# Kernel tuning notes

Hardware: AMD Instinct MI355X
Metric: run time of the kernel (lower is better)

Reference implementation:

```python
import jax, jax.numpy as jnp
import numpy as np

B, T, C = 4, 1024, 512
H, HD = 8, 64
NE, K = 8, 2
FF = 4 * C


def setup_inputs() -> dict:
    key = jax.random.key(0)
    ks = jax.random.split(key, 16)
    s = 0.02
    return {
        "x": jax.random.normal(ks[0], (B, T, C), jnp.float32),
        "ln1_g": jnp.ones((C,), jnp.float32),
        "ln1_b": jnp.zeros((C,), jnp.float32),
        "ln2_g": jnp.ones((C,), jnp.float32),
        "ln2_b": jnp.zeros((C,), jnp.float32),
        "Wq": jax.random.normal(ks[1], (H, C, HD), jnp.float32) * s,
        "Wk": jax.random.normal(ks[2], (H, C, HD), jnp.float32) * s,
        "Wv": jax.random.normal(ks[3], (H, C, HD), jnp.float32) * s,
        "Wp": jax.random.normal(ks[4], (H * HD, C), jnp.float32) * s,
        "bp": jnp.zeros((C,), jnp.float32),
        "Wr": jax.random.normal(ks[5], (C, NE), jnp.float32) * s,
        "br": jnp.zeros((NE,), jnp.float32),
        "W1": jax.random.normal(ks[6], (NE, C, FF), jnp.float32) * s,
        "b1": jnp.zeros((NE, FF), jnp.float32),
        "W2": jax.random.normal(ks[7], (NE, FF, C), jnp.float32) * s,
        "b2": jnp.zeros((NE, C), jnp.float32),
    }


def _ln(x, g, b, eps=1e-5):
    mu = jnp.mean(x, axis=-1, keepdims=True)
    var = jnp.var(x, axis=-1, keepdims=True)
    return (x - mu) * jax.lax.rsqrt(var + eps) * g + b


def reference(x, ln1_g, ln1_b, ln2_g, ln2_b, Wq, Wk, Wv, Wp, bp, Wr, br, W1, b1, W2, b2):
    # --- multi-head causal attention (all heads stacked) ---
    h = _ln(x, ln1_g, ln1_b)
    q = jnp.einsum("btc,hcd->bhtd", h, Wq)
    k = jnp.einsum("btc,hcd->bhtd", h, Wk)
    v = jnp.einsum("btc,hcd->bhtd", h, Wv)
    wei = jnp.einsum("bhtd,bhsd->bhts", q, k) / np.sqrt(HD).astype(np.float32)
    causal = jnp.tril(jnp.ones((T, T), bool))
    wei = jnp.where(causal, wei, -jnp.inf)
    wei = jax.nn.softmax(wei, axis=-1)
    attn = jnp.einsum("bhts,bhsd->bhtd", wei, v)  # [B,H,T,HD]
    attn = attn.transpose(0, 2, 1, 3).reshape(B, T, H * HD)
    x2 = x + attn @ Wp + bp

    # --- SparseMoE: dense all-experts compute, masked top-k combine ---
    h2 = _ln(x2, ln2_g, ln2_b)
    scores = h2 @ Wr + br  # [B,T,NE]
    topk_scores, indices = jax.lax.top_k(scores, K)
    # scatter top-k scores into zeros (rest stays 0), then softmax over experts
    mask = jnp.sum(jax.nn.one_hot(indices, NE, dtype=scores.dtype) * topk_scores[..., None], axis=-2)
    router = jax.nn.softmax(mask, axis=-1)  # [B,T,NE]
    hid = jax.nn.relu(jnp.einsum("btc,ecf->btef", h2, W1) + b1)  # [B,T,NE,FF]
    eo = jnp.einsum("btef,efc->btec", hid, W2) + b2  # [B,T,NE,C]
    moe = jnp.einsum("bte,btec->btc", router, eo)
    return x2 + moe
```

## Files before the change

kernel.cpp:

```cpp
#include <hip/hip_runtime.h>


typedef unsigned short u16;
typedef __attribute__((ext_vector_type(8))) short s16x8;
typedef __attribute__((ext_vector_type(4))) float f32x4;

__device__ __forceinline__ u16 f2bf(float f) {
  union { float f; unsigned u; } v; v.f = f;
  unsigned r = v.u + 0x7fffu + ((v.u >> 16) & 1u);
  return (u16)(r >> 16);
}
__device__ __forceinline__ float bf2f(u16 h) {
  union { unsigned u; float f; } v; v.u = ((unsigned)h) << 16;
  return v.f;
}

#define GLDS16(g, s) __builtin_amdgcn_global_load_lds( \
    (const __attribute__((address_space(1))) void*)(g), \
    (__attribute__((address_space(3))) void*)(s), 16, 0, 0)

#define MFMA16(a, b, c) __builtin_amdgcn_mfma_f32_16x16x32_bf16((a), (b), (c), 0, 0, 0)

__global__ __launch_bounds__(256) void transpose_k(
    const float* __restrict__ in, u16* __restrict__ out,
    int R, int C, long long ibs, long long obs, float scale)
{
  __shared__ float tile[32][33];
  in  += (long long)blockIdx.z * ibs;
  out += (long long)blockIdx.z * obs;
  const int c0 = blockIdx.x * 32, r0 = blockIdx.y * 32;
  const int tx = threadIdx.x, ty = threadIdx.y;
  #pragma unroll
  for (int i = 0; i < 4; ++i)
    tile[ty + i*8][tx] = in[(size_t)(r0 + ty + i*8) * C + c0 + tx];
  __syncthreads();
  #pragma unroll
  for (int i = 0; i < 4; ++i)
    out[(size_t)(c0 + ty + i*8) * R + r0 + tx] = f2bf(tile[tx][ty + i*8] * scale);
}

__global__ __launch_bounds__(256) void transqkv_k(
    const float* __restrict__ Wq, const float* __restrict__ Wk,
    const float* __restrict__ Wv, const float* __restrict__ Wp,
    u16* __restrict__ oqkv, u16* __restrict__ owp)
{
  __shared__ float tile[32][33];
  const int z = blockIdx.z;
  const int tx = threadIdx.x, ty = threadIdx.y;
  if (z < 24) {
    const int which = z >> 3, head = z & 7;
    const float* in = (which == 0 ? Wq : (which == 1 ? Wk : Wv)) + (size_t)head * 512 * 64;
    u16* o = oqkv + (size_t)which * 512 * 512 + (size_t)head * 64 * 512;
    const float scale = (which == 0) ? 0.125f : 1.f;
    const int c0 = blockIdx.x * 32, r0 = blockIdx.y * 32;
    #pragma unroll
    for (int i = 0; i < 4; ++i)
      tile[ty + i*8][tx] = in[(size_t)(r0 + ty + i*8) * 64 + c0 + tx];
    __syncthreads();
    #pragma unroll
    for (int i = 0; i < 4; ++i)
      o[(size_t)(c0 + ty + i*8) * 512 + r0 + tx] = f2bf(tile[tx][ty + i*8] * scale);
  } else {
    const int zz = z - 24;
    const int c0 = (zz * 2 + blockIdx.x) * 32;
    const int r0 = blockIdx.y * 32;
    #pragma unroll
    for (int i = 0; i < 4; ++i)
      tile[ty + i*8][tx] = Wp[(size_t)(r0 + ty + i*8) * 512 + c0 + tx];
    __syncthreads();
    #pragma unroll
    for (int i = 0; i < 4; ++i)
      owp[(size_t)(c0 + ty + i*8) * 512 + r0 + tx] = f2bf(tile[tx][ty + i*8]);
  }
}

__global__ __launch_bounds__(256) void vtrans_k(
    const u16* __restrict__ qkv, u16* __restrict__ vt)
{
  __shared__ u16 tile[32][33];
  const int bh = blockIdx.z, b = bh >> 3, h = bh & 7;
  const int t0 = blockIdx.x * 32, d0 = blockIdx.y * 32;
  const int tx = threadIdx.x, ty = threadIdx.y;
  #pragma unroll
  for (int i = 0; i < 4; ++i)
    tile[ty + i*8][tx] = qkv[(size_t)(b*1024 + t0 + ty + i*8) * 1536 + 1024 + h*64 + d0 + tx];
  __syncthreads();
  #pragma unroll
  for (int i = 0; i < 4; ++i)
    vt[(size_t)bh*65536 + (size_t)(d0 + ty + i*8) * 1024 + t0 + tx] = tile[tx][ty + i*8];
}

__global__ __launch_bounds__(256) void ln_k(
    const float* __restrict__ x, const float* __restrict__ g,
    const float* __restrict__ b, u16* __restrict__ o)
{
  const int row = blockIdx.x, t = threadIdx.x;
  const float* xr = x + (size_t)row * 512;
  const float a0 = xr[t], a1 = xr[t + 256];
  float s = a0 + a1, ss = a0*a0 + a1*a1;
  #pragma unroll
  for (int off = 1; off < 64; off <<= 1) {
    s  += __shfl_xor(s, off);
    ss += __shfl_xor(ss, off);
  }
  __shared__ float rs[4], rq[4];
  const int w = t >> 6;
  if ((t & 63) == 0) { rs[w] = s; rq[w] = ss; }
  __syncthreads();
  s  = rs[0] + rs[1] + rs[2] + rs[3];
  ss = rq[0] + rq[1] + rq[2] + rq[3];
  const float mu = s * (1.f/512.f);
  const float var = ss * (1.f/512.f) - mu*mu;
  const float rstd = rsqrtf(var + 1e-5f);
  o[(size_t)row*512 + t]       = f2bf((a0 - mu) * rstd * g[t]     + b[t]);
  o[(size_t)row*512 + t + 256] = f2bf((a1 - mu) * rstd * g[t+256] + b[t+256]);
}

template<int BN, int EPI>
__global__ __launch_bounds__(256) void gemm2p(
    const u16* __restrict__ A, const u16* __restrict__ Bt,
    int M, int N, int K, int lda, int ldb,
    u16* __restrict__ obf, float* __restrict__ oa,
    const float* __restrict__ bias, const float* __restrict__ extra, int e0)
{
  constexpr int NB = BN / 32;
  constexpr int SB = BN / 32;
  __shared__ u16 Asm[2][128*64];
  __shared__ u16 Bsm[2][BN*64];
  const int t = threadIdx.x, l = t & 63;
  const int wid = t >> 6, wr = wid >> 1, wc = wid & 1;
  const int lrow = l & 15, lhi = l >> 4;
  const int m0 = blockIdx.x * 128, n0 = blockIdx.y * BN;

  const f32x4 z4 = {0.f, 0.f, 0.f, 0.f};
  f32x4 acc[4][NB];
  #pragma unroll
  for (int i = 0; i < 4; ++i)
    #pragma unroll
    for (int j = 0; j < NB; ++j) acc[i][j] = z4;

  const u16* ga = A  + (size_t)(m0 + (t >> 3)) * lda + (t & 7) * 8;
  const u16* gb = Bt + (size_t)(n0 + (t >> 3)) * ldb + (t & 7) * 8;

#define STG2(buf, k0) do { \
    _Pragma("unroll") \
    for (int i = 0; i < 4; ++i) \
      GLDS16(ga + (size_t)(i*32)*lda + (k0), (char*)Asm[buf] + i*4096 + t*16); \
    _Pragma("unroll") \
    for (int i = 0; i < SB; ++i) \
      GLDS16(gb + (size_t)(i*32)*ldb + (k0), (char*)Bsm[buf] + i*4096 + t*16); \
  } while (0)

  const int NT = K >> 6;
  STG2(0, 0);
  for (int tt = 0; tt < NT; ++tt) {
    if (tt + 1 < NT) {
      STG2((tt + 1) & 1, (tt + 1) * 64);
      if constexpr (BN == 128) asm volatile("s_waitcnt vmcnt(8)" ::: "memory");
      else                     asm volatile("s_waitcnt vmcnt(6)" ::: "memory");
    } else {
      asm volatile("s_waitcnt vmcnt(0)" ::: "memory");
    }
    __builtin_amdgcn_sched_barrier(0);
    __builtin_amdgcn_s_barrier();
    const u16* As = Asm[tt & 1];
    const u16* Bs = Bsm[tt & 1];
    #pragma unroll
    for (int kh = 0; kh < 2; ++kh) {
      s16x8 af[4], bfr[NB];
      #pragma unroll
      for (int i = 0; i < 4; ++i)
        af[i]  = *(const s16x8*)(As + (wr*64 + i*16 + lrow)*64 + kh*32 + lhi*8);
      #pragma unroll
      for (int j = 0; j < NB; ++j)
        bfr[j] = *(const s16x8*)(Bs + (wc*(BN/2) + j*16 + lrow)*64 + kh*32 + lhi*8);
      #pragma unroll
      for (int i = 0; i < 4; ++i)
        #pragma unroll
        for (int j = 0; j < NB; ++j)
          acc[i][j] = MFMA16(af[i], bfr[j], acc[i][j]);
    }
    __builtin_amdgcn_s_barrier();
    __builtin_amdgcn_sched_barrier(0);
  }
#undef STG2

  #pragma unroll
  for (int i = 0; i < 4; ++i) {
    const int rbase = m0 + wr*64 + i*16 + lhi*4;
    #pragma unroll
    for (int j = 0; j < NB; ++j) {
      const int col = n0 + wc*(BN/2) + j*16 + lrow;
      #pragma unroll
      for (int rr = 0; rr < 4; ++rr) {
        const int row = rbase + rr;
        const float v = acc[i][j][rr];
        if (EPI == 0) {
          obf[(size_t)row*N + col] = f2bf(v);
        } else if (EPI == 1) {
          const float r = extra[(size_t)row*8 + e0 + (col >> 11)];
          obf[(size_t)row*N + col] = f2bf(fmaxf(v + bias[col], 0.f) * r);
        } else {
          oa[(size_t)row*N + col] = v + bias[col] + extra[(size_t)row*N + col];
        }
      }
    }
  }
}

template<int NKT, int EPI>
__global__ __launch_bounds__(512, 2) void gemm8p(
    const u16* __restrict__ A, const u16* __restrict__ Bt,
    int lda, int ldb,
    u16* __restrict__ obf,
    const float* __restrict__ bias, const float* __restrict__ rout)
{
  __shared__ u16 Lds[2][2][256*64];
  const int t = threadIdx.x, l = t & 63;
  const int wid = t >> 6, wm = wid >> 2, wn = wid & 3;
  const int lrow = l & 15, lhi = l >> 4;

  int m0, n0, zz = 0;
  {
    const int bid = blockIdx.x;
    const int r = bid & 7, k = bid >> 3;
    if (EPI == 1) {
      m0 = (k >> 3) * 256; n0 = (r * 8 + (k & 7)) * 256;
    } else if (EPI == 2) {
      n0 = (r * 8 + (k & 7)) * 256; m0 = (k >> 3) * 256;
    } else if (EPI == 4) {
      zz = r*4 + (k & 3);
      const int mn = k >> 2;
      m0 = (mn >> 1) * 256; n0 = (mn & 1) * 256;
    } else {
      zz = r*2 + (k & 1);
      const int mn = k >> 1;
      m0 = (mn >> 1) * 256; n0 = (mn & 1) * 256;
    }
  }
  constexpr int KCH = (EPI == 4) ? 512 : 1024;
  const u16* Ab = A  + (size_t)m0 * lda + ((EPI == 4 || EPI == 5) ? zz * KCH : 0);
  const u16* Bb = Bt + (size_t)n0 * ldb + ((EPI == 4 || EPI == 5) ? zz * KCH : 0);

  const int tr = t >> 3;
  const int sc = ((t & 7) ^ (tr & 7)) * 8;

#define STGU(bf, kt, op_, u4_) do { \
    const u16* s_ = (op_) ? Bb : Ab; \
    const int ld_ = (op_) ? ldb : lda; \
    GLDS16(s_ + (size_t)((u4_)*64 + tr) * ld_ + (size_t)(kt)*64 + sc, \
           (char*)&Lds[bf][op_][0] + (u4_)*8192 + t*16); \
  } while (0)

#define RD(Ls, row, kb) (*(const s16x8*)((const char*)(Ls) + (row)*128 + ((kb) ^ (((row)&7)<<4))))

  f32x4 acc[8][4];
  const f32x4 z4 = {0.f, 0.f, 0.f, 0.f};
  #pragma unroll
  for (int i = 0; i < 8; ++i)
    #pragma unroll
    for (int j = 0; j < 4; ++j) acc[i][j] = z4;

  #pragma unroll
  for (int u = 0; u < 4; ++u) STGU(0, 0, 0, u);
  #pragma unroll
  for (int u = 0; u < 4; ++u) STGU(0, 0, 1, u);
  if (NKT > 1) {
    #pragma unroll
    for (int u = 0; u < 4; ++u) STGU(1, 1, 1, u);
    asm volatile("s_waitcnt vmcnt(4)" ::: "memory");
  } else {
    asm volatile("s_waitcnt vmcnt(0)" ::: "memory");
  }
  __builtin_amdgcn_sched_barrier(0);
  __builtin_amdgcn_s_barrier();

  s16x8 frA[2][4], frB[2][4];
  #pragma unroll 2
  for (int X = 0; X < NKT; ++X) {
    const u16* As = &Lds[X & 1][0][0];
    const u16* Bs = &Lds[X & 1][1][0];
    #pragma unroll
    for (int kk = 0; kk < 2; ++kk) {
      #pragma unroll
      for (int nf = 0; nf < 4; ++nf)
        frB[kk][nf] = RD(Bs, wn*64 + nf*16 + lrow, kk*64 + lhi*16);
      #pragma unroll
      for (int mf = 0; mf < 4; ++mf)
        frA[kk][mf] = RD(As, wm*128 + mf*16 + lrow, kk*64 + lhi*16);
    }
    if (X + 1 < NKT) {
      #pragma unroll
      for (int u = 0; u < 4; ++u) STGU((X + 1) & 1, X + 1, 0, u);
    }
    __builtin_amdgcn_s_barrier();
    asm volatile("s_waitcnt lgkmcnt(0)" ::: "memory");
    __builtin_amdgcn_sched_barrier(0);
    __builtin_amdgcn_s_setprio(1);
    #pragma unroll
    for (int kk = 0; kk < 2; ++kk)
      #pragma unroll
      for (int mf = 0; mf < 4; ++mf)
        #pragma unroll
        for (int nf = 0; nf < 4; ++nf)
          acc[mf][nf] = MFMA16(frA[kk][mf], frB[kk][nf], acc[mf][nf]);
    __builtin_amdgcn_s_setprio(0);
    __builtin_amdgcn_s_barrier();
    #pragma unroll
    for (int kk = 0; kk < 2; ++kk)
      #pragma unroll
      for (int mf = 0; mf < 4; ++mf)
        frA[kk][mf] = RD(As, wm*128 + 64 + mf*16 + lrow, kk*64 + lhi*16);
    if (X + 2 < NKT) {
      #pragma unroll
      for (int u = 0; u < 4; ++u) STGU(X & 1, X + 2, 1, u);
    }
    __builtin_amdgcn_s_barrier();
    asm volatile("s_waitcnt lgkmcnt(0)" ::: "memory");
    __builtin_amdgcn_sched_barrier(0);
    __builtin_amdgcn_s_setprio(1);
    #pragma unroll
    for (int kk = 0; kk < 2; ++kk)
      #pragma unroll
      for (int mf = 0; mf < 4; ++mf)
        #pragma unroll
        for (int nf = 0; nf < 4; ++nf)
          acc[4 + mf][nf] = MFMA16(frA[kk][mf], frB[kk][nf], acc[4 + mf][nf]);
    __builtin_amdgcn_s_setprio(0);
    if (X + 1 < NKT) {
      if (X + 2 < NKT) asm volatile("s_waitcnt vmcnt(4)" ::: "memory");
      else             asm volatile("s_waitcnt vmcnt(0)" ::: "memory");
      __builtin_amdgcn_sched_barrier(0);
    }
    __builtin_amdgcn_s_barrier();
  }
#undef STGU
#undef RD

  constexpr size_t PSTRIDE = (EPI == 4) ? (size_t)1024*512 : (size_t)2048*512;
  u16* outp = (EPI == 4 || EPI == 5) ? obf + (size_t)zz * PSTRIDE : obf;
  const int Nld = (EPI == 1 || EPI == 2) ? 16384 : 512;
  #pragma unroll
  for (int mf = 0; mf < 8; ++mf) {
    const int rbase = m0 + wm*128 + mf*16 + lhi*4;
    #pragma unroll
    for (int nf = 0; nf < 4; ++nf) {
      const int col = n0 + wn*64 + nf*16 + lrow;
      #pragma unroll
      for (int rr = 0; rr < 4; ++rr) {
        const int row = rbase + rr;
        float v = acc[mf][nf][rr];
        if (EPI == 1 || EPI == 2) {
          const float r = rout[(size_t)row*8 + (col >> 11)];
          outp[(size_t)row*16384 + col] = f2bf(fmaxf(v + bias[col], 0.f) * r);
        } else {
          outp[(size_t)row*512 + col] = f2bf(v);
        }
      }
    }
  }
}

template<int Z>
__global__ __launch_bounds__(256) void combineZ_k(
    float* __restrict__ outq, const u16* __restrict__ P, size_t pstride,
    const float* __restrict__ routq, const float* __restrict__ b2)
{
  const int row = blockIdx.x, t = threadIdx.x;
  const int c = t * 2;
  float r[8];
  #pragma unroll
  for (int e = 0; e < 8; ++e) r[e] = routq[(size_t)row*8 + e];
  float v0 = outq[(size_t)row*512 + c];
  float v1 = outq[(size_t)row*512 + c + 1];
  #pragma unroll
  for (int z = 0; z < Z; ++z) {
    const unsigned pv = *(const unsigned*)(P + (size_t)z*pstride + (size_t)row*512 + c);
    v0 += bf2f((u16)(pv & 0xffffu));
    v1 += bf2f((u16)(pv >> 16));
  }
  #pragma unroll
  for (int e = 0; e < 8; ++e) {
    v0 += r[e] * b2[(size_t)e*512 + c];
    v1 += r[e] * b2[(size_t)e*512 + c + 1];
  }
  outq[(size_t)row*512 + c]     = v0;
  outq[(size_t)row*512 + c + 1] = v1;
}

__global__ __launch_bounds__(256) void gemm2_k(
    const u16* __restrict__ hid, const u16* __restrict__ w2t,
    u16* __restrict__ P, int e0, int accum)
{
  __shared__ u16 Asm[128*64];
  __shared__ u16 Bsm[64*64];
  const int t = threadIdx.x;
  const int l = t & 63;
  const int wid = t >> 6, wr = wid >> 1, wc = wid & 1;
  const int lrow = l & 15, lhi = l >> 4;
  const int m0 = blockIdx.x * 128, n0 = blockIdx.y * 64, z = blockIdx.z;

  const u16* A  = hid + z * 2048;
  const u16* Bt = w2t + (size_t)(e0 + z) * 512 * 2048;
  u16* Pz = P + (size_t)z * 4096 * 512;

  const f32x4 z4 = {0.f, 0.f, 0.f, 0.f};
  f32x4 acc[4][2];
  #pragma unroll
  for (int i = 0; i < 4; ++i) { acc[i][0] = z4; acc[i][1] = z4; }

  const u16* ga = A  + (size_t)(m0 + (t >> 3)) * 4096 + (t & 7) * 8;
  const u16* gb = Bt + (size_t)(n0 + (t >> 3)) * 2048 + (t & 7) * 8;

  for (int k0 = 0; k0 < 2048; k0 += 64) {
    #pragma unroll
    for (int i = 0; i < 4; ++i)
      GLDS16(ga + (size_t)i*32*4096 + k0, (char*)Asm + i*4096 + t*16);
    #pragma unroll
    for (int i = 0; i < 2; ++i)
      GLDS16(gb + (size_t)i*32*2048 + k0, (char*)Bsm + i*4096 + t*16);
    __syncthreads();
    #pragma unroll
    for (int kh = 0; kh < 2; ++kh) {
      s16x8 af[4], bfr[2];
      #pragma unroll
      for (int i = 0; i < 4; ++i)
        af[i]  = *(const s16x8*)(Asm + (wr*64 + i*16 + lrow)*64 + kh*32 + lhi*8);
      #pragma unroll
      for (int j = 0; j < 2; ++j)
        bfr[j] = *(const s16x8*)(Bsm + (wc*32 + j*16 + lrow)*64 + kh*32 + lhi*8);
      #pragma unroll
      for (int i = 0; i < 4; ++i)
        #pragma unroll
        for (int j = 0; j < 2; ++j)
          acc[i][j] = MFMA16(af[i], bfr[j], acc[i][j]);
    }
    __syncthreads();
  }

  #pragma unroll
  for (int i = 0; i < 4; ++i) {
    const int rbase = m0 + wr*64 + i*16 + lhi*4;
    #pragma unroll
    for (int j = 0; j < 2; ++j) {
      const int col = n0 + wc*32 + j*16 + lrow;
      #pragma unroll
      for (int rr = 0; rr < 4; ++rr) {
        const size_t idx = (size_t)(rbase + rr) * 512 + col;
        const float old = accum ? bf2f(Pz[idx]) : 0.f;
        Pz[idx] = f2bf(old + acc[i][j][rr]);
      }
    }
  }
}

__global__ __launch_bounds__(256) void combineB_k(
    float* __restrict__ out, const u16* __restrict__ P,
    const float* __restrict__ rout, const float* __restrict__ b2)
{
  const int row = blockIdx.x, t = threadIdx.x;
  float r[8];
  #pragma unroll
  for (int e = 0; e < 8; ++e) r[e] = rout[(size_t)row*8 + e];
  #pragma unroll
  for (int cc = 0; cc < 2; ++cc) {
    const int c = t + cc*256;
    const size_t idx = (size_t)row*512 + c;
    float v = out[idx] + bf2f(P[idx]) + bf2f(P[(size_t)4096*512 + idx]);
    #pragma unroll
    for (int e = 0; e < 8; ++e) v += r[e] * b2[(size_t)e*512 + c];
    out[idx] = v;
  }
}

__global__ __launch_bounds__(256) void attn_k(
    const u16* __restrict__ qkv, const u16* __restrict__ vt, u16* __restrict__ o)
{
  const int bid = blockIdx.x;
  const int xcd = bid & 7, rr_ = bid >> 3;
  const int bh = (rr_ >> 3) * 8 + xcd;
  const int qp = rr_ & 7;
  const int b = bh >> 3, h = bh & 7;
  const int t = threadIdx.x, l = t & 63, w = t >> 6;
  const int lrow = l & 15, lhi = l >> 4;

  __shared__ u16 Ksm[2][64*64];
  __shared__ u16 Vsm[2][64*64];
  __shared__ u16 Psm[4][16][72];

  const int trow = t >> 3;
  const int csw = ((t & 7) ^ (trow & 7)) * 8;
  const u16* gk = qkv + (size_t)(b*1024 + trow) * 1536 + 512 + h*64 + csw;
  const u16* gv = vt + (size_t)bh*65536 + (size_t)trow*1024 + csw;
  const f32x4 z4 = {0.f,0.f,0.f,0.f};

#define ASTAGE(buf, s0) do { \
    _Pragma("unroll") \
    for (int i = 0; i < 2; ++i) { \
      GLDS16(gk + (size_t)((s0) + i*32) * 1536, (char*)Ksm[buf] + i*4096 + t*16); \
      GLDS16(gv + (s0) + (size_t)(i*32)*1024,   (char*)Vsm[buf] + i*4096 + t*16); \
    } } while (0)

  for (int pass = 0; pass < 2; ++pass) {
    const int qb = pass ? (15 - qp) : qp;
    const int t0w = qb*64 + w*16;
    const u16* qrow = qkv + (size_t)(b*1024 + t0w + lrow) * 1536 + h*64 + lhi*8;
    s16x8 qf0 = *(const s16x8*)qrow;
    s16x8 qf1 = *(const s16x8*)(qrow + 32);

    float m[4], sl[4];
    f32x4 oacc[4];
    #pragma unroll
    for (int i = 0; i < 4; ++i) { m[i] = -1e30f; sl[i] = 0.f; oacc[i] = z4; }

    const int nt = qb + 1;
    ASTAGE(0, 0);
    for (int kv = 0; kv < nt; ++kv) {
      const int s0 = kv * 64;
      if (kv + 1 < nt) {
        ASTAGE((kv + 1) & 1, s0 + 64);
        asm volatile("s_waitcnt vmcnt(4)" ::: "memory");
      } else {
        asm volatile("s_waitcnt vmcnt(0)" ::: "memory");
      }
      __builtin_amdgcn_s_barrier();
      __builtin_amdgcn_sched_barrier(0);
      const u16* Ks = Ksm[kv & 1];
      const u16* Vs = Vsm[kv & 1];

      f32x4 sacc[4] = {z4, z4, z4, z4};
      #pragma unroll
      for (int n = 0; n < 4; ++n) {
        const int r = n*16 + lrow;
        s16x8 kf0 = *(const s16x8*)((const char*)Ks + r*128 + ((lhi*16) ^ ((r & 7) << 4)));
        s16x8 kf1 = *(const s16x8*)((const char*)Ks + r*128 + ((64 + lhi*16) ^ ((r & 7) << 4)));
        sacc[n] = MFMA16(qf0, kf0, sacc[n]);
        sacc[n] = MFMA16(qf1, kf1, sacc[n]);
      }
      if (s0 + 63 > t0w) {
        #pragma unroll
        for (int n = 0; n < 4; ++n)
          #pragma unroll
          for (int rr = 0; rr < 4; ++rr)
            if (s0 + n*16 + lrow > t0w + lhi*4 + rr) sacc[n][rr] = -1e30f;
      }
      float pm[4];
      #pragma unroll
      for (int rr = 0; rr < 4; ++rr)
        pm[rr] = fmaxf(fmaxf(sacc[0][rr], sacc[1][rr]), fmaxf(sacc[2][rr], sacc[3][rr]));
      #pragma unroll
      for (int rr = 0; rr < 4; ++rr) {
        pm[rr] = fmaxf(pm[rr], __shfl_xor(pm[rr], 1));
        pm[rr] = fmaxf(pm[rr], __shfl_xor(pm[rr], 2));
        pm[rr] = fmaxf(pm[rr], __shfl_xor(pm[rr], 4));
        pm[rr] = fmaxf(pm[rr], __shfl_xor(pm[rr], 8));
      }
      float p[4][4], ps[4], scv[4];
      #pragma unroll
      for (int rr = 0; rr < 4; ++rr) {
        const float mn = fmaxf(m[rr], pm[rr]);
        scv[rr] = __expf(m[rr] - mn);
        m[rr] = mn;
        ps[rr] = 0.f;
        #pragma unroll
        for (int n = 0; n < 4; ++n) {
          p[n][rr] = __expf(sacc[n][rr] - mn);
          ps[rr] += p[n][rr];
        }
      }
      #pragma unroll
      for (int rr = 0; rr < 4; ++rr) {
        ps[rr] += __shfl_xor(ps[rr], 1);
        ps[rr] += __shfl_xor(ps[rr], 2);
        ps[rr] += __shfl_xor(ps[rr], 4);
        ps[rr] += __shfl_xor(ps[rr], 8);
        sl[rr] = sl[rr] * scv[rr] + ps[rr];
      }
      #pragma unroll
      for (int ct = 0; ct < 4; ++ct) {
        f32x4 t4 = oacc[ct];
        #pragma unroll
        for (int rr = 0; rr < 4; ++rr) t4[rr] *= scv[rr];
        oacc[ct] = t4;
      }
      #pragma unroll
      for (int n = 0; n < 4; ++n)
        #pragma unroll
        for (int rr = 0; rr < 4; ++rr)
          Psm[w][lhi*4 + rr][n*16 + lrow] = f2bf(p[n][rr]);
      asm volatile("s_waitcnt lgkmcnt(0)" ::: "memory");
      __builtin_amdgcn_sched_barrier(0);
      s16x8 pa0 = *(const s16x8*)&Psm[w][lrow][lhi*8];
      s16x8 pa1 = *(const s16x8*)&Psm[w][lrow][32 + lhi*8];
      #pragma unroll
      for (int ct = 0; ct < 4; ++ct) {
        const int r = ct*16 + lrow;
        s16x8 vb0 = *(const s16x8*)((const char*)Vs + r*128 + ((lhi*16) ^ ((r & 7) << 4)));
        s16x8 vb1 = *(const s16x8*)((const char*)Vs + r*128 + ((64 + lhi*16) ^ ((r & 7) << 4)));
        oacc[ct] = MFMA16(pa0, vb0, oacc[ct]);
        oacc[ct] = MFMA16(pa1, vb1, oacc[ct]);
      }
      __builtin_amdgcn_s_barrier();
      __builtin_amdgcn_sched_barrier(0);
    }
    #pragma unroll
    for (int ct = 0; ct < 4; ++ct)
      #pragma unroll
      for (int rr = 0; rr < 4; ++rr) {
        const int row = b*1024 + t0w + lhi*4 + rr;
        o[(size_t)row*512 + h*64 + ct*16 + lrow] = f2bf(oacc[ct][rr] / sl[rr]);
      }
  }
#undef ASTAGE
}

__global__ __launch_bounds__(256) void router_k(
    const float* __restrict__ x2, const float* __restrict__ g,
    const float* __restrict__ b, const float* __restrict__ Wr,
    const float* __restrict__ br, float* __restrict__ rt,
    u16* __restrict__ h2o)
{
  const int l = threadIdx.x & 63, w = threadIdx.x >> 6;
  const int tkn = blockIdx.x * 4 + w;
  const float* xr = x2 + (size_t)tkn * 512;
  float v[8];
  float s = 0.f, ss = 0.f;
  #pragma unroll
  for (int i = 0; i < 8; ++i) {
    v[i] = xr[l*8 + i];
    s += v[i]; ss += v[i]*v[i];
  }
  #pragma unroll
  for (int off = 1; off < 64; off <<= 1) {
    s  += __shfl_xor(s, off);
    ss += __shfl_xor(ss, off);
  }
  const float mu = s * (1.f/512.f);
  const float var = ss * (1.f/512.f) - mu*mu;
  const float rstd = rsqrtf(var + 1e-5f);
  float acc[8];
  #pragma unroll
  for (int e = 0; e < 8; ++e) acc[e] = 0.f;
  s16x8 hw;
  #pragma unroll
  for (int i = 0; i < 8; ++i) {
    const int c = l*8 + i;
    const float hv = (v[i] - mu) * rstd * g[c] + b[c];
    hw[i] = (short)f2bf(hv);
    const float* wrow = Wr + (size_t)c * 8;
    #pragma unroll
    for (int e = 0; e < 8; ++e) acc[e] += hv * wrow[e];
  }
  *(s16x8*)(h2o + (size_t)tkn*512 + l*8) = hw;
  #pragma unroll
  for (int e = 0; e < 8; ++e) {
    #pragma unroll
    for (int off = 1; off < 64; off <<= 1) acc[e] += __shfl_xor(acc[e], off);
    acc[e] += br[e];
  }
  int e1 = 0;
  #pragma unroll
  for (int e = 1; e < 8; ++e) if (acc[e] > acc[e1]) e1 = e;
  int e2 = (e1 == 0) ? 1 : 0;
  #pragma unroll
  for (int e = 0; e < 8; ++e) if (e != e1 && acc[e] > acc[e2]) e2 = e;
  const float mx = fmaxf(acc[e1], 0.f);
  float Z = 0.f;
  #pragma unroll
  for (int e = 0; e < 8; ++e) {
    const float mv = (e == e1 || e == e2) ? acc[e] : 0.f;
    Z += __expf(mv - mx);
  }
  if (l < 8) {
    const float mv = (l == e1 || l == e2) ? acc[l] : 0.f;
    rt[(size_t)tkn * 8 + l] = __expf(mv - mx) / Z;
  }
}

extern "C" void kernel_launch(void* const* d_in, const int* in_sizes, int n_in,
                              void* d_out, int out_size, void* d_ws, size_t ws_size,
                              hipStream_t stream) {
  const float* x    = (const float*)d_in[0];
  const float* ln1g = (const float*)d_in[1];
  const float* ln1b = (const float*)d_in[2];
  const float* ln2g = (const float*)d_in[3];
  const float* ln2b = (const float*)d_in[4];
  const float* Wq   = (const float*)d_in[5];
  const float* Wk   = (const float*)d_in[6];
  const float* Wv   = (const float*)d_in[7];
  const float* Wp   = (const float*)d_in[8];
  const float* bp   = (const float*)d_in[9];
  const float* Wr   = (const float*)d_in[10];
  const float* br   = (const float*)d_in[11];
  const float* W1   = (const float*)d_in[12];
  const float* b1   = (const float*)d_in[13];
  const float* W2   = (const float*)d_in[14];
  const float* b2   = (const float*)d_in[15];
  float* out = (float*)d_out;

  const int pathH = (ws_size >= (size_t)138543104) ? 1 : 0;
  const int pathN = (ws_size >= (size_t)104988672) ? 1 : 0;

  char* ws = (char*)d_ws;
  size_t off = 0;
  auto alloc = [&](size_t bytes) -> char* {
    char* p = ws + off;
    off += (bytes + 255) & ~(size_t)255;
    return p;
  };
  u16* w1_t = (u16*)alloc((size_t)8*2048*512*2);
  u16* w2f  = (u16*)alloc((size_t)8*512*2048*2);
  u16* h2b  = (u16*)alloc((size_t)4096*512*2);
  float* rout = (float*)alloc((size_t)4096*8*4);
  u16* hidq = (u16*)alloc(pathH ? (size_t)2048*16384*2 : (size_t)4096*4096*2);
  u16* Ppl  = (u16*)alloc(pathH ? (size_t)16*2048*512*2
                                : (pathN ? (size_t)32*1024*512*2 : (size_t)2*4096*512*2));
  u16* wqkv_t = (u16*)hidq;
  u16* wp_t   = (u16*)((char*)hidq + 1572864);
  u16* hb     = (u16*)((char*)hidq + 2097152);
  u16* attnb  = (u16*)((char*)hidq + 6291456);
  u16* qkvb   = (u16*)((char*)hidq + 10485760);
  u16* vtb    = (u16*)((char*)hidq + 23068672);

  const dim3 tb(32, 8);
  transqkv_k<<<dim3(2,16,32), tb, 0, stream>>>(Wq, Wk, Wv, Wp, wqkv_t, wp_t);
  transpose_k<<<dim3(64,16,8), tb, 0, stream>>>(W1, w1_t, 512, 2048, (long long)512*2048, (long long)2048*512, 1.f);
  if (pathN)
    transpose_k<<<dim3(16,512,1), tb, 0, stream>>>(W2, w2f, 16384, 512, 0, 0, 1.f);
  else
    transpose_k<<<dim3(16,64,8), tb, 0, stream>>>(W2, w2f, 2048, 512, (long long)2048*512, (long long)512*2048, 1.f);

  ln_k<<<4096, 256, 0, stream>>>(x, ln1g, ln1b, hb);
  gemm2p<128,0><<<dim3(32,12), 256, 0, stream>>>(hb, wqkv_t, 4096, 1536, 512, 512, 512,
                                                 qkvb, nullptr, nullptr, nullptr, 0);
  vtrans_k<<<dim3(32,2,32), tb, 0, stream>>>(qkvb, vtb);
  attn_k<<<256, 256, 0, stream>>>(qkvb, vtb, attnb);
  gemm2p<64,2><<<dim3(32,8), 256, 0, stream>>>(attnb, wp_t, 4096, 512, 512, 512, 512,
                                               nullptr, out, bp, x, 0);
  router_k<<<1024, 256, 0, stream>>>(out, ln2g, ln2b, Wr, br, rout, h2b);

  if (pathH) {
    for (int h = 0; h < 2; ++h) {
      gemm8p<8,2><<<512, 512, 0, stream>>>(h2b + (size_t)h*2048*512, w1_t, 512, 512,
                                           hidq, b1, rout + (size_t)h*16384);
      gemm8p<16,5><<<256, 512, 0, stream>>>(hidq, w2f, 16384, 16384,
                                            Ppl, nullptr, nullptr);
      combineZ_k<16><<<2048, 256, 0, stream>>>(out + (size_t)h*2048*512, Ppl,
                                               (size_t)2048*512,
                                               rout + (size_t)h*16384, b2);
    }
  } else if (pathN) {
    for (int q = 0; q < 4; ++q) {
      gemm8p<8,1><<<256, 512, 0, stream>>>(h2b + (size_t)q*1024*512, w1_t, 512, 512,
                                           hidq, b1, rout + (size_t)q*8192);
      gemm8p<8,4><<<256, 512, 0, stream>>>(hidq, w2f, 16384, 16384,
                                           Ppl, nullptr, nullptr);
      combineZ_k<32><<<1024, 256, 0, stream>>>(out + (size_t)q*1024*512, Ppl,
                                               (size_t)1024*512,
                                               rout + (size_t)q*8192, b2);
    }
  } else {
    for (int p = 0; p < 4; ++p) {
      const int e0 = 2*p;
      gemm2p<128,1><<<dim3(32,32), 256, 0, stream>>>(h2b, w1_t + (size_t)e0*2048*512,
                                                     4096, 4096, 512, 512, 512,
                                                     hidq, nullptr, b1 + (size_t)e0*2048, rout, e0);
      gemm2_k<<<dim3(32,8,2), 256, 0, stream>>>(hidq, w2f, Ppl, e0, p > 0 ? 1 : 0);
    }
    combineB_k<<<4096, 256, 0, stream>>>(out, Ppl, rout, b2);
  }
}
```

Baseline: 278.6 us.

## Replace 256x256 gemm8p MoE path with 128-tile gemm2p and 8-way split-K

On the pathH branch, the two large 256x256-tile gemm8p kernels for the MoE expert FFN are replaced by the smaller 128-tile gemm2p kernel. The second GEMM now uses an 8-way split-K over blockIdx.z, writing bf16 partials that combineZ<8> reduces, instead of the previous 16-way split. A new EPI==3 epilogue is added to gemm2p, and the now-unused EPI 2/5 variants of gemm8p are removed. The goal is better occupancy and tile balance and fewer partial buffers to reduce, at the cost of less data reuse per tile.

```diff
diff --git a/kernel.cpp b/kernel.cpp
--- a/kernel.cpp
+++ b/kernel.cpp
@@ -132,6 +132,13 @@
   const int lrow = l & 15, lhi = l >> 4;
   const int m0 = blockIdx.x * 128, n0 = blockIdx.y * BN;
 
+  const u16* Ab = A;
+  const u16* Bb = Bt;
+  if (EPI == 3) {
+    Ab += (size_t)blockIdx.z * 2048;
+    Bb += (size_t)blockIdx.z * 2048;
+  }
+
   const f32x4 z4 = {0.f, 0.f, 0.f, 0.f};
   f32x4 acc[4][NB];
   #pragma unroll
@@ -139,8 +146,8 @@
     #pragma unroll
     for (int j = 0; j < NB; ++j) acc[i][j] = z4;
 
-  const u16* ga = A  + (size_t)(m0 + (t >> 3)) * lda + (t & 7) * 8;
-  const u16* gb = Bt + (size_t)(n0 + (t >> 3)) * ldb + (t & 7) * 8;
+  const u16* ga = Ab + (size_t)(m0 + (t >> 3)) * lda + (t & 7) * 8;
+  const u16* gb = Bb + (size_t)(n0 + (t >> 3)) * ldb + (t & 7) * 8;
 
 #define STG2(buf, k0) do { \
     _Pragma("unroll") \
@@ -200,8 +207,11 @@
         } else if (EPI == 1) {
           const float r = extra[(size_t)row*8 + e0 + (col >> 11)];
           obf[(size_t)row*N + col] = f2bf(fmaxf(v + bias[col], 0.f) * r);
+        } else if (EPI == 2) {
+          oa[(size_t)row*N + col] = v + bias[col] + extra[(size_t)row*N + col];
         } else {
-          oa[(size_t)row*N + col] = v + bias[col] + extra[(size_t)row*N + col];
+          u16* outp = obf + (size_t)blockIdx.z * M * 512;
+          outp[(size_t)row*512 + col] = f2bf(v);
         }
       }
     }
@@ -226,21 +236,15 @@
     const int r = bid & 7, k = bid >> 3;
     if (EPI == 1) {
       m0 = (k >> 3) * 256; n0 = (r * 8 + (k & 7)) * 256;
-    } else if (EPI == 2) {
-      n0 = (r * 8 + (k & 7)) * 256; m0 = (k >> 3) * 256;
-    } else if (EPI == 4) {
+    } else {
       zz = r*4 + (k & 3);
       const int mn = k >> 2;
       m0 = (mn >> 1) * 256; n0 = (mn & 1) * 256;
-    } else {
-      zz = r*2 + (k & 1);
-      const int mn = k >> 1;
-      m0 = (mn >> 1) * 256; n0 = (mn & 1) * 256;
-    }
-  }
-  constexpr int KCH = (EPI == 4) ? 512 : 1024;
-  const u16* Ab = A  + (size_t)m0 * lda + ((EPI == 4 || EPI == 5) ? zz * KCH : 0);
-  const u16* Bb = Bt + (size_t)n0 * ldb + ((EPI == 4 || EPI == 5) ? zz * KCH : 0);
+    }
+  }
+  constexpr int KCH = 512;
+  const u16* Ab = A  + (size_t)m0 * lda + ((EPI == 4) ? zz * KCH : 0);
+  const u16* Bb = Bt + (size_t)n0 * ldb + ((EPI == 4) ? zz * KCH : 0);
 
   const int tr = t >> 3;
   const int sc = ((t & 7) ^ (tr & 7)) * 8;
@@ -337,9 +341,8 @@
 #undef STGU
 #undef RD
 
-  constexpr size_t PSTRIDE = (EPI == 4) ? (size_t)1024*512 : (size_t)2048*512;
-  u16* outp = (EPI == 4 || EPI == 5) ? obf + (size_t)zz * PSTRIDE : obf;
-  const int Nld = (EPI == 1 || EPI == 2) ? 16384 : 512;
+  u16* outp = (EPI == 4) ? obf + (size_t)zz * 1024 * 512 : obf;
+  const int Nld = (EPI == 1) ? 16384 : 512;
   #pragma unroll
   for (int mf = 0; mf < 8; ++mf) {
     const int rbase = m0 + wm*128 + mf*16 + lhi*4;
@@ -350,7 +353,7 @@
       for (int rr = 0; rr < 4; ++rr) {
         const int row = rbase + rr;
         float v = acc[mf][nf][rr];
-        if (EPI == 1 || EPI == 2) {
+        if (EPI == 1) {
           const float r = rout[(size_t)row*8 + (col >> 11)];
           outp[(size_t)row*16384 + col] = f2bf(fmaxf(v + bias[col], 0.f) * r);
         } else {
@@ -741,13 +744,15 @@
 
   if (pathH) {
     for (int h = 0; h < 2; ++h) {
-      gemm8p<8,2><<<512, 512, 0, stream>>>(h2b + (size_t)h*2048*512, w1_t, 512, 512,
-                                           hidq, b1, rout + (size_t)h*16384);
-      gemm8p<16,5><<<256, 512, 0, stream>>>(hidq, w2f, 16384, 16384,
-                                            Ppl, nullptr, nullptr);
-      combineZ_k<16><<<2048, 256, 0, stream>>>(out + (size_t)h*2048*512, Ppl,
-                                               (size_t)2048*512,
-                                               rout + (size_t)h*16384, b2);
+      gemm2p<128,1><<<dim3(16,128), 256, 0, stream>>>(
+          h2b + (size_t)h*2048*512, w1_t, 2048, 16384, 512, 512, 512,
+          hidq, nullptr, b1, rout + (size_t)h*16384, 0);
+      gemm2p<128,3><<<dim3(16,4,8), 256, 0, stream>>>(
+          hidq, w2f, 2048, 512, 2048, 16384, 16384,
+          Ppl, nullptr, nullptr, nullptr, 0);
+      combineZ_k<8><<<2048, 256, 0, stream>>>(out + (size_t)h*2048*512, Ppl,
+                                              (size_t)2048*512,
+                                              rout + (size_t)h*16384, b2);
     }
   } else if (pathN) {
     for (int q = 0; q < 4; ++q) {
```

Measured after the change: 317.5 us. +14.0%, slower.
